# Optimization experiments

Hardware: AMD Instinct MI355X
Metric: run time of the kernel (lower is better)

## Reference

```python
import jax, jax.numpy as jnp
import numpy as np

EMBED_DIM = 1024
N_HEADS = 16
HEAD_DIM = EMBED_DIM // N_HEADS
B, S = 2, 2048


def setup_inputs() -> dict:
    key = jax.random.key(0)
    ks = jax.random.split(key, 10)
    x = jax.random.normal(ks[0], (B, S, EMBED_DIM), dtype=jnp.float32)
    # binary KG mask; force diagonal to 1 so every query attends to >=1 key
    kg_mask = jax.random.randint(ks[1], (B, S, S), 0, 2).astype(jnp.float32)
    kg_mask = kg_mask.at[:, jnp.arange(S), jnp.arange(S)].set(1.0)
    scale = 1.0 / np.sqrt(EMBED_DIM)
    def lin(k):
        return jax.random.normal(k, (EMBED_DIM, EMBED_DIM), dtype=jnp.float32) * scale
    return {
        'x': x, 'kg_mask': kg_mask,
        'Wq': lin(ks[2]), 'bq': jnp.zeros((EMBED_DIM,), jnp.float32),
        'Wk': lin(ks[3]), 'bk': jnp.zeros((EMBED_DIM,), jnp.float32),
        'Wv': lin(ks[4]), 'bv': jnp.zeros((EMBED_DIM,), jnp.float32),
        'Wo': lin(ks[5]), 'bo': jnp.zeros((EMBED_DIM,), jnp.float32),
    }


def reference(x, kg_mask, Wq, bq, Wk, bk, Wv, bv, Wo, bo):
    b, s, d = x.shape
    h, hd = N_HEADS, HEAD_DIM
    # projections -> (b, h, s, hd)
    def proj(W, bias):
        y = jnp.einsum('bsd,de->bse', x, W) + bias
        return y.reshape(b, s, h, hd).transpose(0, 2, 1, 3)
    Q, K, V = proj(Wq, bq), proj(Wk, bk), proj(Wv, bv)
    scores = jnp.einsum('bhqd,bhkd->bhqk', Q, K) / np.sqrt(hd).astype(jnp.float32)
    scores = jnp.where(kg_mask[:, None, :, :] == 0, -jnp.inf, scores)
    attn = jax.nn.softmax(scores, axis=-1)
    out = jnp.einsum('bhqk,bhkd->bhqd', attn, V)
    out = out.transpose(0, 2, 1, 3).reshape(b, s, d)
    return jnp.einsum('bsd,de->bse', out, Wo) + bo
```

## Files before the change

kernel.cpp:

```cpp
#include <hip/hip_runtime.h>
#include <hip/hip_bf16.h>


#define SEQ 2048
#define SCEXP 0.18033688011112043f

typedef __attribute__((ext_vector_type(8))) short short8;
typedef __attribute__((ext_vector_type(4))) float f32x4;

union S8U {
    short8 s;
    unsigned u[4];
};

__device__ __forceinline__ unsigned short f2b(float f) {
    unsigned u = __builtin_bit_cast(unsigned, f);
    u += 0x7fffu + ((u >> 16) & 1u);
    return (unsigned short)(u >> 16);
}

__device__ __forceinline__ unsigned pk2(float a, float b) {
    __hip_bfloat162 h = __float22bfloat162_rn(float2{a, b});
    unsigned r;
    __builtin_memcpy(&r, &h, 4);
    return r;
}

__global__ __launch_bounds__(256) void xcvt(const float* __restrict__ X,
                                            unsigned short* __restrict__ Xb) {
    const size_t base = ((size_t)blockIdx.x * 256 + threadIdx.x) * 8;
    f32x4 v0 = *(const f32x4*)&X[base];
    f32x4 v1 = *(const f32x4*)&X[base + 4];
    S8U o;
    o.u[0] = pk2(v0[0], v0[1]);
    o.u[1] = pk2(v0[2], v0[3]);
    o.u[2] = pk2(v1[0], v1[1]);
    o.u[3] = pk2(v1[2], v1[3]);
    *(short8*)&Xb[base] = o.s;
}

__global__ __launch_bounds__(256) void wcvt(const float* __restrict__ W0, const float* __restrict__ W1,
                                            const float* __restrict__ W2, const float* __restrict__ W3,
                                            unsigned short* __restrict__ T0, unsigned short* __restrict__ T1,
                                            unsigned short* __restrict__ T2, unsigned short* __restrict__ T3) {
    const float* W = blockIdx.z == 0 ? W0 : blockIdx.z == 1 ? W1 : blockIdx.z == 2 ? W2 : W3;
    unsigned short* T = blockIdx.z == 0 ? T0 : blockIdx.z == 1 ? T1 : blockIdx.z == 2 ? T2 : T3;
    const float sc = (blockIdx.z == 0) ? SCEXP : 1.f;
    __shared__ float Ls[64][65];
    const int tid = threadIdx.x;
    const int n0 = blockIdx.x * 64, k0 = blockIdx.y * 64;
#pragma unroll
    for (int i = 0; i < 4; ++i) {
        int q = tid + i * 256; int k = q >> 4, c = q & 15;
        f32x4 v = *(const f32x4*)&W[(size_t)(k0 + k) * 1024 + n0 + c * 4];
        Ls[k][c * 4 + 0] = v[0]; Ls[k][c * 4 + 1] = v[1];
        Ls[k][c * 4 + 2] = v[2]; Ls[k][c * 4 + 3] = v[3];
    }
    __syncthreads();
#pragma unroll
    for (int i = 0; i < 2; ++i) {
        int q = tid + i * 256; int n = q >> 3, c = q & 7;
        short8 ov;
#pragma unroll
        for (int j = 0; j < 8; ++j) ov[j] = (short)f2b(Ls[c * 8 + j][n] * sc);
        *(short8*)&T[(size_t)(n0 + n) * 1024 + k0 + c * 8] = ov;
    }
}

__global__ __launch_bounds__(256) void vtr(const unsigned short* __restrict__ V,
                                           unsigned short* __restrict__ Vt) {
    __shared__ __align__(16) unsigned short Ls[64][80];
    const int tid = threadIdx.x;
    const int s0 = blockIdx.x * 64;
    const size_t base = (size_t)blockIdx.y * SEQ * 64;
#pragma unroll
    for (int i = 0; i < 2; ++i) {
        int q = tid + i * 256; int s = q >> 3, c = q & 7;
        *(short8*)&Ls[s][c * 8] = *(const short8*)&V[base + (size_t)(s0 + s) * 64 + c * 8];
    }
    __syncthreads();
#pragma unroll
    for (int i = 0; i < 2; ++i) {
        int q = tid + i * 256; int e = q >> 3, c = q & 7;
        short8 ov;
#pragma unroll
        for (int j = 0; j < 8; ++j) ov[j] = (short)Ls[c * 8 + j][e];
        *(short8*)&Vt[base + (size_t)e * SEQ + s0 + c * 8] = ov;
    }
}

#define CHE ((size_t)4096 * 1024)

template <int MODE>
__global__ __launch_bounds__(256) void gemm_mfma(const unsigned short* __restrict__ Ab,
                                                 const unsigned short* __restrict__ Bt,
                                                 const float* __restrict__ b0,
                                                 const float* __restrict__ b1,
                                                 const float* __restrict__ b2,
                                                 void* __restrict__ Yp) {
    __shared__ __align__(16) char AsB[8192];
    __shared__ __align__(16) char BsB[8192];
    const int tid = threadIdx.x;
    const int w = tid >> 6, l = tid & 63, lo = l & 15, hi = l >> 4;
    const int m0 = blockIdx.y * 128, n0 = blockIdx.x * 128;
    const int wm = (w & 1) * 64, wn = (w >> 1) * 64;
    const int which = (MODE == 1) ? (n0 >> 10) : 0;
    const float* biasp = which == 0 ? b0 : which == 1 ? b1 : b2;
    const float bsc = (MODE == 1 && which == 0) ? SCEXP : 1.f;

    f32x4 acc[4][4];
#pragma unroll
    for (int i = 0; i < 4; ++i)
#pragma unroll
        for (int j = 0; j < 4; ++j) acc[i][j] = f32x4{0.f, 0.f, 0.f, 0.f};

    const int cm = tid >> 2, cc = tid & 3;
    short8 fa8[2], fb[2];
    auto FETCH = [&](int kk) {
#pragma unroll
        for (int i = 0; i < 2; ++i) {
            int m = cm + 64 * i;
            fa8[i] = *(const short8*)&Ab[(size_t)(m0 + m) * 1024 + kk + cc * 8];
            fb[i] = *(const short8*)&Bt[(size_t)(n0 + m) * 1024 + kk + cc * 8];
        }
    };

    FETCH(0);
    for (int k0 = 0; k0 < 1024; k0 += 32) {
#pragma unroll
        for (int i = 0; i < 2; ++i) {
            int m = cm + 64 * i;
            int dst = (m * 64 + cc * 16) ^ ((m & 7) << 4);
            *(short8*)(AsB + dst) = fa8[i];
            *(short8*)(BsB + dst) = fb[i];
        }
        __syncthreads();
        if (k0 + 32 < 1024) FETCH(k0 + 32);

        short8 af_[4], bf_[4];
#pragma unroll
        for (int t = 0; t < 4; ++t) {
            int r = wm + t * 16 + lo;
            af_[t] = *(const short8*)(AsB + ((r * 64 + hi * 16) ^ ((r & 7) << 4)));
            int rn = wn + t * 16 + lo;
            bf_[t] = *(const short8*)(BsB + ((rn * 64 + hi * 16) ^ ((rn & 7) << 4)));
        }
        __builtin_amdgcn_s_setprio(1);
#pragma unroll
        for (int mt = 0; mt < 4; ++mt)
#pragma unroll
            for (int nt = 0; nt < 4; ++nt)
                acc[mt][nt] = __builtin_amdgcn_mfma_f32_16x16x32_bf16(af_[mt], bf_[nt], acc[mt][nt], 0, 0, 0);
        __builtin_amdgcn_s_setprio(0);
        __syncthreads();
    }

    float bv[4];
#pragma unroll
    for (int nt = 0; nt < 4; ++nt)
        bv[nt] = biasp[(n0 & 1023) + wn + nt * 16 + lo] * bsc;
#pragma unroll
    for (int mt = 0; mt < 4; ++mt)
#pragma unroll
        for (int nt = 0; nt < 4; ++nt)
#pragma unroll
            for (int r = 0; r < 4; ++r) {
                float v = acc[mt][nt][r] + bv[nt];
                int m = m0 + wm + mt * 16 + hi * 4 + r;
                int nloc = (n0 & 1023) + wn + nt * 16 + lo;
                if (MODE == 1) {
                    int b = m >> 11, s = m & 2047, hh = nloc >> 6, e = nloc & 63;
                    ((unsigned short*)Yp)[(size_t)which * CHE + (size_t)((b * 16 + hh) * SEQ + s) * 64 + e] = f2b(v);
                } else {
                    ((float*)Yp)[(size_t)m * 1024 + nloc] = v;
                }
            }
}

__global__ __launch_bounds__(256) void attn_mfma(const unsigned short* __restrict__ Qg,
                                                 const unsigned short* __restrict__ Kg,
                                                 const unsigned short* __restrict__ Vtg,
                                                 const float* __restrict__ mask,
                                                 unsigned short* __restrict__ Og) {
    __shared__ __align__(16) char KsB[8192];
    __shared__ __align__(16) char VsB[8192];
    __shared__ __align__(16) char PsB[8192];
    const int tid = threadIdx.x;
    const int w = tid >> 6, l = tid & 63, lo = l & 15, hi = l >> 4;
    const int qt = blockIdx.x, bh = blockIdx.y, b = bh >> 4, h = bh & 15;

    const unsigned short* Qp = Qg + ((size_t)bh * SEQ + qt * 64 + w * 16 + lo) * 64;
    const short8 qf0 = *(const short8*)(Qp + hi * 8);
    const short8 qf1 = *(const short8*)(Qp + 32 + hi * 8);
    const unsigned short* Kb = Kg + (size_t)bh * SEQ * 64;
    const unsigned short* Vb = Vtg + (size_t)bh * 64 * SEQ;
    const float* mrow = mask + (size_t)b * SEQ * SEQ + (size_t)(qt * 64 + w * 16 + lo) * SEQ;
    char* PsW = PsB + w * 2048;

    float m_run = -1e30f, l_run = 0.f;
    const float MASKED = -2e30f;
    f32x4 acc[4];
#pragma unroll
    for (int nt = 0; nt < 4; ++nt) acc[nt] = f32x4{0.f, 0.f, 0.f, 0.f};

    const int sk = tid >> 3, scol = tid & 7;
    short8 pk[2], pv[2];
    f32x4 pm[4];
    auto FETCH = [&](int kv) {
#pragma unroll
        for (int i = 0; i < 2; ++i) {
            int row = sk + 32 * i;
            pk[i] = *(const short8*)&Kb[(size_t)(kv * 64 + row) * 64 + scol * 8];
            pv[i] = *(const short8*)&Vb[(size_t)row * SEQ + kv * 64 + scol * 8];
        }
#pragma unroll
        for (int kt = 0; kt < 4; ++kt)
            pm[kt] = *(const f32x4*)&mrow[kv * 64 + kt * 16 + hi * 4];
    };

    FETCH(0);
    for (int kv = 0; kv < 32; ++kv) {
#pragma unroll
        for (int i = 0; i < 2; ++i) {
            int row = sk + 32 * i;
            int dst = (row * 128 + scol * 16) ^ ((row & 7) << 4);
            *(short8*)(KsB + dst) = pk[i];
            *(short8*)(VsB + dst) = pv[i];
        }
        f32x4 mv[4];
#pragma unroll
        for (int kt = 0; kt < 4; ++kt) mv[kt] = pm[kt];
        __syncthreads();
        if (kv + 1 < 32) FETCH(kv + 1);

        f32x4 st[4];
        __builtin_amdgcn_s_setprio(1);
#pragma unroll
        for (int kt = 0; kt < 4; ++kt) {
            int r = kt * 16 + lo;
            short8 kf0 = *(const short8*)(KsB + ((r * 128 + hi * 16) ^ ((lo & 7) << 4)));
            short8 kf1 = *(const short8*)(KsB + ((r * 128 + 64 + hi * 16) ^ ((lo & 7) << 4)));
            f32x4 z = {0.f, 0.f, 0.f, 0.f};
            z = __builtin_amdgcn_mfma_f32_16x16x32_bf16(kf0, qf0, z, 0, 0, 0);
            st[kt] = __builtin_amdgcn_mfma_f32_16x16x32_bf16(kf1, qf1, z, 0, 0, 0);
        }
        __builtin_amdgcn_s_setprio(0);

        float pmax = MASKED;
#pragma unroll
        for (int kt = 0; kt < 4; ++kt)
#pragma unroll
            for (int r = 0; r < 4; ++r) {
                float sv = (mv[kt][r] == 0.f) ? MASKED : st[kt][r];
                st[kt][r] = sv;
                pmax = fmaxf(pmax, sv);
            }
        pmax = fmaxf(pmax, __shfl_xor(pmax, 16, 64));
        pmax = fmaxf(pmax, __shfl_xor(pmax, 32, 64));

        if (!__all(pmax <= m_run + 8.f)) {
            float mnew = fmaxf(m_run, pmax);
            float scf = __builtin_amdgcn_exp2f(m_run - mnew);
            l_run *= scf;
            float scr[4];
#pragma unroll
            for (int r = 0; r < 4; ++r) scr[r] = __shfl(scf, (hi << 2) + r, 64);
#pragma unroll
            for (int nt = 0; nt < 4; ++nt)
#pragma unroll
                for (int r = 0; r < 4; ++r) acc[nt][r] *= scr[r];
            m_run = mnew;
        }

        float sum = 0.f;
        unsigned wpk[4][2];
#pragma unroll
        for (int kt = 0; kt < 4; ++kt) {
            float p0 = __builtin_amdgcn_exp2f(st[kt][0] - m_run);
            float p1 = __builtin_amdgcn_exp2f(st[kt][1] - m_run);
            float p2 = __builtin_amdgcn_exp2f(st[kt][2] - m_run);
            float p3 = __builtin_amdgcn_exp2f(st[kt][3] - m_run);
            sum += (p0 + p1) + (p2 + p3);
            wpk[kt][0] = pk2(p0, p1);
            wpk[kt][1] = pk2(p2, p3);
        }
        sum += __shfl_xor(sum, 16, 64);
        sum += __shfl_xor(sum, 32, 64);
        l_run += sum;

#pragma unroll
        for (int kt = 0; kt < 4; ++kt) {
            int d0 = (lo * 128 + kt * 32 + hi * 8) ^ ((lo & 7) << 4);
            *(unsigned*)(PsW + d0) = wpk[kt][0];
            *(unsigned*)(PsW + d0 + 4) = wpk[kt][1];
        }
        short8 pa0 = *(const short8*)(PsW + ((lo * 128 + hi * 16) ^ ((lo & 7) << 4)));
        short8 pa1 = *(const short8*)(PsW + ((lo * 128 + 64 + hi * 16) ^ ((lo & 7) << 4)));
        __builtin_amdgcn_s_setprio(1);
#pragma unroll
        for (int nt = 0; nt < 4; ++nt) {
            int r = nt * 16 + lo;
            short8 v0 = *(const short8*)(VsB + ((r * 128 + hi * 16) ^ ((lo & 7) << 4)));
            short8 v1 = *(const short8*)(VsB + ((r * 128 + 64 + hi * 16) ^ ((lo & 7) << 4)));
            acc[nt] = __builtin_amdgcn_mfma_f32_16x16x32_bf16(pa0, v0, acc[nt], 0, 0, 0);
            acc[nt] = __builtin_amdgcn_mfma_f32_16x16x32_bf16(pa1, v1, acc[nt], 0, 0, 0);
        }
        __builtin_amdgcn_s_setprio(0);
        __syncthreads();
    }

    float lr[4];
#pragma unroll
    for (int r = 0; r < 4; ++r) lr[r] = 1.f / __shfl(l_run, (hi << 2) + r, 64);
#pragma unroll
    for (int nt = 0; nt < 4; ++nt)
#pragma unroll
        for (int r = 0; r < 4; ++r) {
            int qg2 = qt * 64 + w * 16 + hi * 4 + r;
            Og[(size_t)(b * SEQ + qg2) * 1024 + h * 64 + nt * 16 + lo] = f2b(acc[nt][r] * lr[r]);
        }
}

extern "C" void kernel_launch(void* const* d_in, const int* in_sizes, int n_in,
                              void* d_out, int out_size, void* d_ws, size_t ws_size,
                              hipStream_t stream) {
    const float* x  = (const float*)d_in[0];
    const float* kg = (const float*)d_in[1];
    const float* Wq = (const float*)d_in[2];
    const float* bq = (const float*)d_in[3];
    const float* Wk = (const float*)d_in[4];
    const float* bk = (const float*)d_in[5];
    const float* Wv = (const float*)d_in[6];
    const float* bv = (const float*)d_in[7];
    const float* Wo = (const float*)d_in[8];
    const float* bo = (const float*)d_in[9];

    unsigned short* ws = (unsigned short*)d_ws;
    const size_t WSZ = 1024 * 1024;
    unsigned short* wtq = ws;
    unsigned short* wtk = ws + WSZ;
    unsigned short* wtv = ws + 2 * WSZ;
    unsigned short* wto = ws + 3 * WSZ;
    unsigned short* xb  = ws + 4 * WSZ;
    unsigned short* qb  = ws + 8 * WSZ;
    unsigned short* kb  = qb + CHE;
    unsigned short* vb  = kb + CHE;
    unsigned short* vt  = vb + CHE;
    unsigned short* ob  = vt + CHE;

    xcvt<<<2048, 256, 0, stream>>>(x, xb);
    wcvt<<<dim3(16, 16, 4), 256, 0, stream>>>(Wq, Wk, Wv, Wo, wtq, wtk, wtv, wto);

    gemm_mfma<1><<<dim3(24, 32), 256, 0, stream>>>(xb, wtq, bq, bk, bv, qb);

    vtr<<<dim3(32, 32), 256, 0, stream>>>(vb, vt);

    attn_mfma<<<dim3(32, 32), 256, 0, stream>>>(qb, kb, vt, kg, ob);

    gemm_mfma<0><<<dim3(8, 32), 256, 0, stream>>>(ob, wto, bo, bo, bo, d_out);
}
```

Measured before the change: 275.2 us.

## Double-buffer K/V tiles in LDS and widen attention blocks to 128 queries

```diff
diff --git a/kernel.cpp b/kernel.cpp
--- a/kernel.cpp
+++ b/kernel.cpp
@@ -177,24 +177,24 @@
             }
 }
 
-__global__ __launch_bounds__(256) void attn_mfma(const unsigned short* __restrict__ Qg,
+__global__ __launch_bounds__(512) void attn_mfma(const unsigned short* __restrict__ Qg,
                                                  const unsigned short* __restrict__ Kg,
                                                  const unsigned short* __restrict__ Vtg,
                                                  const float* __restrict__ mask,
                                                  unsigned short* __restrict__ Og) {
-    __shared__ __align__(16) char KsB[8192];
-    __shared__ __align__(16) char VsB[8192];
-    __shared__ __align__(16) char PsB[8192];
+    __shared__ __align__(16) char KsB[2][8192];
+    __shared__ __align__(16) char VsB[2][8192];
+    __shared__ __align__(16) char PsB[16384];
     const int tid = threadIdx.x;
     const int w = tid >> 6, l = tid & 63, lo = l & 15, hi = l >> 4;
     const int qt = blockIdx.x, bh = blockIdx.y, b = bh >> 4, h = bh & 15;
 
-    const unsigned short* Qp = Qg + ((size_t)bh * SEQ + qt * 64 + w * 16 + lo) * 64;
+    const unsigned short* Qp = Qg + ((size_t)bh * SEQ + qt * 128 + w * 16 + lo) * 64;
     const short8 qf0 = *(const short8*)(Qp + hi * 8);
     const short8 qf1 = *(const short8*)(Qp + 32 + hi * 8);
     const unsigned short* Kb = Kg + (size_t)bh * SEQ * 64;
     const unsigned short* Vb = Vtg + (size_t)bh * 64 * SEQ;
-    const float* mrow = mask + (size_t)b * SEQ * SEQ + (size_t)(qt * 64 + w * 16 + lo) * SEQ;
+    const float* mrow = mask + (size_t)b * SEQ * SEQ + (size_t)(qt * 128 + w * 16 + lo) * SEQ;
     char* PsW = PsB + w * 2048;
 
     float m_run = -1e30f, l_run = 0.f;
@@ -204,33 +204,29 @@
     for (int nt = 0; nt < 4; ++nt) acc[nt] = f32x4{0.f, 0.f, 0.f, 0.f};
 
     const int sk = tid >> 3, scol = tid & 7;
-    short8 pk[2], pv[2];
+    const int sdst = (sk * 128 + scol * 16) ^ ((sk & 7) << 4);
+    short8 pk, pv;
     f32x4 pm[4];
     auto FETCH = [&](int kv) {
-#pragma unroll
-        for (int i = 0; i < 2; ++i) {
-            int row = sk + 32 * i;
-            pk[i] = *(const short8*)&Kb[(size_t)(kv * 64 + row) * 64 + scol * 8];
-            pv[i] = *(const short8*)&Vb[(size_t)row * SEQ + kv * 64 + scol * 8];
-        }
+        pk = *(const short8*)&Kb[(size_t)(kv * 64 + sk) * 64 + scol * 8];
+        pv = *(const short8*)&Vb[(size_t)sk * SEQ + kv * 64 + scol * 8];
 #pragma unroll
         for (int kt = 0; kt < 4; ++kt)
             pm[kt] = *(const f32x4*)&mrow[kv * 64 + kt * 16 + hi * 4];
     };
 
     FETCH(0);
+    *(short8*)(KsB[0] + sdst) = pk;
+    *(short8*)(VsB[0] + sdst) = pv;
+    __syncthreads();
+
     for (int kv = 0; kv < 32; ++kv) {
-#pragma unroll
-        for (int i = 0; i < 2; ++i) {
-            int row = sk + 32 * i;
-            int dst = (row * 128 + scol * 16) ^ ((row & 7) << 4);
-            *(short8*)(KsB + dst) = pk[i];
-            *(short8*)(VsB + dst) = pv[i];
-        }
+        const int cur = kv & 1;
+        const char* Kc = KsB[cur];
+        const char* Vc = VsB[cur];
         f32x4 mv[4];
 #pragma unroll
         for (int kt = 0; kt < 4; ++kt) mv[kt] = pm[kt];
-        __syncthreads();
         if (kv + 1 < 32) FETCH(kv + 1);
 
         f32x4 st[4];
@@ -238,8 +234,8 @@
 #pragma unroll
         for (int kt = 0; kt < 4; ++kt) {
             int r = kt * 16 + lo;
-            short8 kf0 = *(const short8*)(KsB + ((r * 128 + hi * 16) ^ ((lo & 7) << 4)));
-            short8 kf1 = *(const short8*)(KsB + ((r * 128 + 64 + hi * 16) ^ ((lo & 7) << 4)));
+            short8 kf0 = *(const short8*)(Kc + ((r * 128 + hi * 16) ^ ((lo & 7) << 4)));
+            short8 kf1 = *(const short8*)(Kc + ((r * 128 + 64 + hi * 16) ^ ((lo & 7) << 4)));
             f32x4 z = {0.f, 0.f, 0.f, 0.f};
             z = __builtin_amdgcn_mfma_f32_16x16x32_bf16(kf0, qf0, z, 0, 0, 0);
             st[kt] = __builtin_amdgcn_mfma_f32_16x16x32_bf16(kf1, qf1, z, 0, 0, 0);
@@ -300,12 +296,17 @@
 #pragma unroll
         for (int nt = 0; nt < 4; ++nt) {
             int r = nt * 16 + lo;
-            short8 v0 = *(const short8*)(VsB + ((r * 128 + hi * 16) ^ ((lo & 7) << 4)));
-            short8 v1 = *(const short8*)(VsB + ((r * 128 + 64 + hi * 16) ^ ((lo & 7) << 4)));
+            short8 v0 = *(const short8*)(Vc + ((r * 128 + hi * 16) ^ ((lo & 7) << 4)));
+            short8 v1 = *(const short8*)(Vc + ((r * 128 + 64 + hi * 16) ^ ((lo & 7) << 4)));
             acc[nt] = __builtin_amdgcn_mfma_f32_16x16x32_bf16(pa0, v0, acc[nt], 0, 0, 0);
             acc[nt] = __builtin_amdgcn_mfma_f32_16x16x32_bf16(pa1, v1, acc[nt], 0, 0, 0);
         }
         __builtin_amdgcn_s_setprio(0);
+
+        if (kv + 1 < 32) {
+            *(short8*)(KsB[cur ^ 1] + sdst) = pk;
+            *(short8*)(VsB[cur ^ 1] + sdst) = pv;
+        }
         __syncthreads();
     }
 
@@ -316,7 +317,7 @@
     for (int nt = 0; nt < 4; ++nt)
 #pragma unroll
         for (int r = 0; r < 4; ++r) {
-            int qg2 = qt * 64 + w * 16 + hi * 4 + r;
+            int qg2 = qt * 128 + w * 16 + hi * 4 + r;
             Og[(size_t)(b * SEQ + qg2) * 1024 + h * 64 + nt * 16 + lo] = f2b(acc[nt][r] * lr[r]);
         }
 }
@@ -355,7 +356,7 @@
 
     vtr<<<dim3(32, 32), 256, 0, stream>>>(vb, vt);
 
-    attn_mfma<<<dim3(32, 32), 256, 0, stream>>>(qb, kb, vt, kg, ob);
+    attn_mfma<<<dim3(16, 32), 512, 0, stream>>>(qb, kb, vt, kg, ob);
 
     gemm_mfma<0><<<dim3(8, 32), 256, 0, stream>>>(ob, wto, bo, bo, bo, d_out);
 }
```

Result: faster. 244.5 us (-11.2%).
